# Kernel tuning notes

Hardware: AMD Instinct MI355X
Metric: run time of the kernel (lower is better)

The kernel has to match this reference:

```python
import jax, jax.numpy as jnp
import numpy as np

HEADS = 4
DIM_HEAD = 32
DIM = 128
HIDDEN = HEADS * DIM_HEAD  # 128
LN_EPS = 1e-6


def setup_inputs() -> dict:
    key = jax.random.key(0)
    ks = jax.random.split(key, 4)
    b, X, Y, Z = 4, 32, 32, 32
    x = jax.random.normal(ks[0], (b, X, Y, Z, DIM), dtype=jnp.float32)
    # 1x1x1 convs are pointwise linears: kernel [in, out]
    w_qkv = jax.random.normal(ks[1], (DIM, 3 * HIDDEN), dtype=jnp.float32) * (DIM ** -0.5)
    w_out = jax.random.normal(ks[2], (HIDDEN, DIM), dtype=jnp.float32) * (HIDDEN ** -0.5)
    b_out = jax.random.normal(ks[3], (DIM,), dtype=jnp.float32) * 0.02
    ln_scale = jnp.ones((DIM,), dtype=jnp.float32)
    ln_bias = jnp.zeros((DIM,), dtype=jnp.float32)
    return {"x": x, "w_qkv": w_qkv, "w_out": w_out, "b_out": b_out,
            "ln_scale": ln_scale, "ln_bias": ln_bias}


def reference(x, w_qkv, w_out, b_out, ln_scale, ln_bias):
    b, X, Y, Z, c = x.shape
    n = X * Y * Z
    scale = DIM_HEAD ** (-0.5)

    # 1x1x1 conv (no bias) == pointwise matmul over channels
    qkv = jnp.einsum('bxyzc,cd->bxyzd', x, w_qkv)  # [b,X,Y,Z,3*hidden]
    q, k, v = jnp.split(qkv, 3, axis=-1)

    # rearrange 'b x y z (h c) -> b h c n'
    def to_bhcn(t):
        return t.reshape(b, n, HEADS, DIM_HEAD).transpose(0, 2, 3, 1)

    q, k, v = to_bhcn(q), to_bhcn(k), to_bhcn(v)

    q = jax.nn.softmax(q, axis=-2) * scale   # softmax over feature dim d
    k = jax.nn.softmax(k, axis=-1)           # softmax over token dim n

    context = jnp.einsum('bhdn,bhcn->bhdc', k, v)   # [b,h,d,c] small d=c=32
    out = jnp.einsum('bhde,bhdn->bhen', context, q) # [b,h,e,n]

    # rearrange 'b h c n -> b x y z (h c)' (cubic volume, matching original)
    out = out.transpose(0, 3, 1, 2).reshape(b, X, Y, Z, HIDDEN)

    # final 1x1x1 conv with bias
    out = jnp.einsum('bxyzh,hc->bxyzc', out, w_out) + b_out

    # LayerNorm over last axis (flax default eps=1e-6, with scale+bias)
    mu = jnp.mean(out, axis=-1, keepdims=True)
    var = jnp.mean(jnp.square(out - mu), axis=-1, keepdims=True)
    out = (out - mu) * jax.lax.rsqrt(var + LN_EPS) * ln_scale + ln_bias
    return out
```

## Files before the change

### kernel.cpp

```cpp
#include <hip/hip_runtime.h>
#include <hip/hip_bf16.h>

typedef _Float16 f16;
typedef _Float16 f16x4 __attribute__((ext_vector_type(4)));
typedef _Float16 f16x8 __attribute__((ext_vector_type(8)));
typedef float f32x4 __attribute__((ext_vector_type(4)));

#define MFMA(a, b, c) __builtin_amdgcn_mfma_f32_16x16x32_f16((a), (b), (c), 0, 0, 0)

#define BB 4
#define NPOS 32768
#define HH 4
#define NBLK 1024
#define NBLK3 2048
#define STATB 2304
#define LDP 136

__device__ __forceinline__ f16x8 ldx8(const float* p) {
  float4 a = *(const float4*)p;
  float4 b = *(const float4*)(p + 4);
  return (f16x8){(f16)a.x, (f16)a.y, (f16)a.z, (f16)a.w,
                 (f16)b.x, (f16)b.y, (f16)b.z, (f16)b.w};
}

__global__ __launch_bounds__(256)
void la_k0_prep(const float* __restrict__ wqkv, f16* __restrict__ wkvF,
                f16* __restrict__ wqF) {
  const int g0 = blockIdx.x * 256 + threadIdx.x;
  for (int i = g0; i < 32768; i += 16384) {
    int j = i & 7, l = (i >> 3) & 63, ks = (i >> 9) & 3, nt = (i >> 11) & 3,
        h = i >> 13;
    int n = 16 * nt + (l & 15);
    int c = 32 * ks + 8 * (l >> 4) + j;
    int col = (n < 32) ? (128 + h * 32 + n) : (256 + h * 32 + (n - 32));
    wkvF[i] = (f16)wqkv[c * 384 + col];
  }
  {
    int i = g0;
    int j = i & 7, l = (i >> 3) & 63, ks = (i >> 9) & 3, a = (i >> 11) & 1,
        h = i >> 12;
    int row = l & 15;
    int n = 8 * (row >> 2) + 4 * a + (row & 3);
    int c = 32 * ks + 8 * (l >> 4) + j;
    wqF[i] = (f16)wqkv[c * 384 + h * 32 + n];
  }
}

__global__ __launch_bounds__(256, 4)
void la_k1_stats(const float* __restrict__ x, const f16* __restrict__ wkvF,
                 char* __restrict__ stats) {
  const int blk = blockIdx.x, t = threadIdx.x;
  const int w = t >> 6, l = t & 63, lg = l >> 4, ln = l & 15;

  __shared__ __align__(16) f16 EV[2][64 * LDP];

  const float* xb = x + (size_t)blk * (128 * 128);
  f16x8 xf[2][4];
#pragma unroll
  for (int mi = 0; mi < 2; ++mi)
#pragma unroll
    for (int ks = 0; ks < 4; ++ks)
      xf[mi][ks] = ldx8(xb + (32 * w + 16 * mi + ln) * 128 + 32 * ks + 8 * lg);

  const f32x4 Z4 = {0.f, 0.f, 0.f, 0.f};

  auto logits = [&](int h, f32x4 (&acc)[2][4]) {
#pragma unroll
    for (int mi = 0; mi < 2; ++mi)
#pragma unroll
      for (int nt = 0; nt < 4; ++nt) acc[mi][nt] = Z4;
#pragma unroll
    for (int ks = 0; ks < 4; ++ks) {
#pragma unroll
      for (int nt = 0; nt < 4; ++nt) {
        f16x8 bf = *(const f16x8*)(wkvF + (((h * 4 + nt) * 4 + ks) << 9) + l * 8);
        acc[0][nt] = MFMA(xf[0][ks], bf, acc[0][nt]);
        acc[1][nt] = MFMA(xf[1][ks], bf, acc[1][nt]);
      }
    }
  };

  auto phaseA = [&](int h, f32x4 (&acc)[2][4]) {
    f16* E = (f16*)EV[h & 1];
    float sl[2] = {0.f, 0.f};
#pragma unroll
    for (int nt = 0; nt < 2; ++nt)
#pragma unroll
      for (int mi = 0; mi < 2; ++mi) {
        float e0 = __expf(acc[mi][nt][0]);
        float e1 = __expf(acc[mi][nt][1]);
        float e2 = __expf(acc[mi][nt][2]);
        float e3 = __expf(acc[mi][nt][3]);
        sl[nt] += (e0 + e1) + (e2 + e3);
        *(f16x4*)&E[(16 * nt + ln) * LDP + 32 * w + 16 * mi + 4 * lg] =
            (f16x4){(f16)e0, (f16)e1, (f16)e2, (f16)e3};
        f32x4 vv = acc[mi][nt + 2];
        *(f16x4*)&E[(32 + 16 * nt + ln) * LDP + 32 * w + 16 * mi + 4 * lg] =
            (f16x4){(f16)vv[0], (f16)vv[1], (f16)vv[2], (f16)vv[3]};
      }
#pragma unroll
    for (int nt = 0; nt < 2; ++nt) {
      sl[nt] += __shfl_xor(sl[nt], 16);
      sl[nt] += __shfl_xor(sl[nt], 32);
    }
    f16* sp = (f16*)(stats + (size_t)(blk * HH + h) * STATB + 2048);
    if (lg == 0) {
      sp[ln * 4 + w] = (f16)sl[0];
      sp[(16 + ln) * 4 + w] = (f16)sl[1];
    }
  };

  auto phaseB = [&](int h) {
    __syncthreads();
    const f16* E = (const f16*)EV[h & 1];
    const int tm = w >> 1, tn = w & 1;
    f32x4 tacc = Z4;
#pragma unroll
    for (int ks = 0; ks < 4; ++ks) {
      f16x8 ea = *(const f16x8*)&E[(16 * tm + ln) * LDP + 32 * ks + 8 * lg];
      f16x8 vb = *(const f16x8*)&E[(32 + 16 * tn + ln) * LDP + 32 * ks + 8 * lg];
      tacc = MFMA(ea, vb, tacc);
    }
    f16* tp = (f16*)(stats + (size_t)(blk * HH + h) * STATB);
#pragma unroll
    for (int r = 0; r < 4; ++r)
      tp[(16 * tm + 4 * lg + r) * 32 + 16 * tn + ln] = (f16)tacc[r];
  };

  f32x4 accA[2][4], accB[2][4];
  logits(0, accA);
  phaseA(0, accA); logits(1, accB); phaseB(0);
  phaseA(1, accB); logits(2, accA); phaseB(1);
  phaseA(2, accA); logits(3, accB); phaseB(2);
  phaseA(3, accB); phaseB(3);
}

__global__ __launch_bounds__(256)
void la_k2_combine(const char* __restrict__ stats, f16* __restrict__ ctxN) {
  const int gid = blockIdx.x;
  const int bh = gid >> 5, d = gid & 31;
  const int b = bh >> 2, h = bh & 3;
  const int t = threadIdx.x, w = t >> 6, l = t & 63;
  const int c = t & 31, grp = t >> 5;
  __shared__ float redt[4][32];
  __shared__ float reds[4];

  float sg = 0.f, tc = 0.f;
  for (int i = grp; i < 256; i += 8) {
    const char* ub = stats + (size_t)((b * 256 + i) * HH + h) * STATB;
    tc += (float)((const f16*)ub)[d * 32 + c];
    f16x4 s4 = *(const f16x4*)(ub + 2048 + d * 8);
    sg += ((float)s4[0] + (float)s4[1]) + ((float)s4[2] + (float)s4[3]);
  }
  tc += __shfl_xor(tc, 32);
  sg += __shfl_xor(sg, 32);
  if (l < 32) redt[w][l] = tc;
  if (l == 0) reds[w] = sg;
  __syncthreads();
  if (t < 32) {
    float tt = (redt[0][t] + redt[1][t]) + (redt[2][t] + redt[3][t]);
    float ss = (reds[0] + reds[1]) + (reds[2] + reds[3]);
    ctxN[((size_t)bh * 32 + d) * 32 + t] = (f16)(tt / ss);
  }
}

__global__ __launch_bounds__(256)
void la_k2b_fold(const f16* __restrict__ ctxN, const float* __restrict__ wout,
                 f16* __restrict__ GTF) {
  const int b = blockIdx.x, t = threadIdx.x;
  const int h = t >> 6, l = t & 63, lg = l >> 4, ln = l & 15;
  const f32x4 Z4 = {0.f, 0.f, 0.f, 0.f};

  const f16* cb = ctxN + (size_t)((b * HH + h) * 32) * 32;
  f16x8 bfrag[2];
#pragma unroll
  for (int nt = 0; nt < 2; ++nt)
    bfrag[nt] = *(const f16x8*)(cb + (16 * nt + ln) * 32 + 8 * lg);

  f16* gf = GTF + (size_t)b * 16384;
#pragma unroll
  for (int mt = 0; mt < 8; ++mt) {
    f16x8 af;
#pragma unroll
    for (int j = 0; j < 8; ++j)
      af[j] = (f16)wout[(32 * h + 8 * lg + j) * 128 + 16 * mt + ln];
#pragma unroll
    for (int nt = 0; nt < 2; ++nt) {
      f32x4 acc = MFMA(af, bfrag[nt], Z4);
#pragma unroll
      for (int r = 0; r < 4; ++r) {
        int dsub = 16 * nt + ln;
        gf[((h * 8 + mt) << 9) + (16 * (dsub >> 3) + 4 * lg + r) * 8 + (dsub & 7)] =
            (f16)acc[r];
      }
    }
  }
}

__global__ __launch_bounds__(256, 2)
void la_k3_out(const float* __restrict__ x, const f16* __restrict__ wqF,
               const f16* __restrict__ GTF, const float* __restrict__ bout,
               const float* __restrict__ lns, const float* __restrict__ lnb,
               float* __restrict__ out) {
  const int blk = blockIdx.x, t = threadIdx.x;
  const int w = t >> 6, l = t & 63, lg = l >> 4, ln = l & 15;
  const int b = blk >> 9;
  const int p0 = blk * 64 + 16 * w;

  const float* xb = x + (size_t)p0 * 128;
  f16x8 xf[4];
#pragma unroll
  for (int ks = 0; ks < 4; ++ks)
    xf[ks] = ldx8(xb + ln * 128 + 32 * ks + 8 * lg);

  const f32x4 Z4 = {0.f, 0.f, 0.f, 0.f};
  const f16* gf = GTF + (size_t)b * 16384;

  f16x8 gA[8], gB[8];
#pragma unroll
  for (int nc = 0; nc < 8; ++nc)
    gA[nc] = *(const f16x8*)(gf + ((0 * 8 + nc) << 9) + l * 8);

  f32x4 y[8];
#pragma unroll
  for (int nc = 0; nc < 8; ++nc) y[nc] = Z4;

  auto qlog = [&](int h, f32x4 (&qa)[2]) {
    qa[0] = Z4;
    qa[1] = Z4;
#pragma unroll
    for (int ks = 0; ks < 4; ++ks) {
      f16x8 a0 = *(const f16x8*)(wqF + (((h * 2 + 0) * 4 + ks) << 9) + l * 8);
      f16x8 a1 = *(const f16x8*)(wqF + (((h * 2 + 1) * 4 + ks) << 9) + l * 8);
      qa[0] = MFMA(a0, xf[ks], qa[0]);
      qa[1] = MFMA(a1, xf[ks], qa[1]);
    }
  };

  auto consume = [&](f32x4 (&qa)[2], f16x8& af) {
    float s = 0.f;
#pragma unroll
    for (int mt = 0; mt < 2; ++mt)
#pragma unroll
      for (int r = 0; r < 4; ++r) {
        qa[mt][r] = __expf(qa[mt][r]);
        s += qa[mt][r];
      }
    s += __shfl_xor(s, 16);
    s += __shfl_xor(s, 32);
    const float inv = 0.17677669529663688f / s;
    af = (f16x8){(f16)(qa[0][0] * inv), (f16)(qa[0][1] * inv),
                 (f16)(qa[0][2] * inv), (f16)(qa[0][3] * inv),
                 (f16)(qa[1][0] * inv), (f16)(qa[1][1] * inv),
                 (f16)(qa[1][2] * inv), (f16)(qa[1][3] * inv)};
  };

  auto prefetch = [&](int h, f16x8 (&g)[8]) {
#pragma unroll
    for (int nc = 0; nc < 8; ++nc)
      g[nc] = *(const f16x8*)(gf + (((h * 8 + nc) << 9) + l * 8));
  };

  auto ymfma = [&](f16x8 (&g)[8], f16x8& af) {
#pragma unroll
    for (int nc = 0; nc < 8; ++nc) y[nc] = MFMA(g[nc], af, y[nc]);
  };

  f32x4 qaA[2], qaB[2];
  f16x8 afA, afB;
  qlog(0, qaA); qlog(1, qaB);
  consume(qaA, afA);
  prefetch(1, gB); ymfma(gA, afA); qlog(2, qaA); consume(qaB, afB);
  prefetch(2, gA); ymfma(gB, afB); qlog(3, qaB); consume(qaA, afA);
  prefetch(3, gB); ymfma(gA, afA); consume(qaB, afB);
  ymfma(gB, afB);

#pragma unroll
  for (int nc = 0; nc < 8; ++nc) {
    f32x4 bb = *(const f32x4*)(bout + 16 * nc + 4 * lg);
    y[nc] += bb;
  }

  float s = 0.f;
#pragma unroll
  for (int nc = 0; nc < 8; ++nc)
    s += (y[nc][0] + y[nc][1]) + (y[nc][2] + y[nc][3]);
  s += __shfl_xor(s, 16);
  s += __shfl_xor(s, 32);
  const float mean = s * (1.f / 128.f);
  float v = 0.f;
#pragma unroll
  for (int nc = 0; nc < 8; ++nc)
#pragma unroll
    for (int r = 0; r < 4; ++r) {
      float dv = y[nc][r] - mean;
      v = fmaf(dv, dv, v);
    }
  v += __shfl_xor(v, 16);
  v += __shfl_xor(v, 32);
  const float inv = rsqrtf(v * (1.f / 128.f) + 1e-6f);

  float* op = out + (size_t)(p0 + ln) * 128;
#pragma unroll
  for (int nc = 0; nc < 8; ++nc) {
    f32x4 sv = *(const f32x4*)(lns + 16 * nc + 4 * lg);
    f32x4 b2 = *(const f32x4*)(lnb + 16 * nc + 4 * lg);
    f32x4 o4;
#pragma unroll
    for (int r = 0; r < 4; ++r)
      o4[r] = (y[nc][r] - mean) * inv * sv[r] + b2[r];
    *(f32x4*)(op + 16 * nc + 4 * lg) = o4;
  }
}

extern "C" void kernel_launch(void* const* d_in, const int* in_sizes, int n_in,
                              void* d_out, int out_size, void* d_ws, size_t ws_size,
                              hipStream_t stream) {
  const float* x = (const float*)d_in[0];
  const float* w_qkv = (const float*)d_in[1];
  const float* w_out = (const float*)d_in[2];
  const float* b_out = (const float*)d_in[3];
  const float* ln_s = (const float*)d_in[4];
  const float* ln_b = (const float*)d_in[5];
  float* out = (float*)d_out;

  char* ws = (char*)d_ws;
  char* stats = ws;
  f16* wkvF = (f16*)(ws + 9437184);
  f16* wqF = (f16*)(ws + 9437184 + 65536);
  f16* GTF = (f16*)(ws + 9437184 + 65536 + 32768);
  f16* ctxN = (f16*)(ws + 9437184 + 65536 + 32768 + 131072);

  la_k0_prep<<<dim3(64), 256, 0, stream>>>(w_qkv, wkvF, wqF);
  la_k1_stats<<<dim3(NBLK), 256, 0, stream>>>(x, wkvF, stats);
  la_k2_combine<<<dim3(512), 256, 0, stream>>>(stats, ctxN);
  la_k2b_fold<<<dim3(BB), 256, 0, stream>>>(ctxN, w_out, GTF);
  la_k3_out<<<dim3(NBLK3), 256, 0, stream>>>(x, wqF, GTF, b_out, ln_s, ln_b, out);
}
```

Before: 87.33 us.

## Use single-wave blocks in output kernel and drop double-buffered G prefetch

The output kernel moves from 256-thread blocks, each covering 64 positions across four waves, to 64-thread single-wave blocks of 16 positions each, so the grid grows fourfold. The explicit double-buffered register prefetch of the folded context/out-projection fragments is removed and each fragment is loaded just before its MFMA. This lowers register pressure and should raise occupancy and scheduling flexibility. The cost is less latency hiding within a wave and more per-block launch overhead.

New measurement: 87.43 us. No clear change (+0.1%).

```diff
diff --git a/kernel.cpp b/kernel.cpp
--- a/kernel.cpp
+++ b/kernel.cpp
@@ -12,7 +12,7 @@
 #define NPOS 32768
 #define HH 4
 #define NBLK 1024
-#define NBLK3 2048
+#define NBLK3 8192
 #define STATB 2304
 #define LDP 136
 
@@ -197,15 +197,15 @@
   }
 }
 
-__global__ __launch_bounds__(256, 2)
+__global__ __launch_bounds__(64)
 void la_k3_out(const float* __restrict__ x, const f16* __restrict__ wqF,
                const f16* __restrict__ GTF, const float* __restrict__ bout,
                const float* __restrict__ lns, const float* __restrict__ lnb,
                float* __restrict__ out) {
-  const int blk = blockIdx.x, t = threadIdx.x;
-  const int w = t >> 6, l = t & 63, lg = l >> 4, ln = l & 15;
-  const int b = blk >> 9;
-  const int p0 = blk * 64 + 16 * w;
+  const int blk = blockIdx.x;
+  const int l = threadIdx.x, lg = l >> 4, ln = l & 15;
+  const int b = blk >> 11;
+  const int p0 = blk * 16;
 
   const float* xb = x + (size_t)p0 * 128;
   f16x8 xf[4];
@@ -215,11 +215,6 @@
 
   const f32x4 Z4 = {0.f, 0.f, 0.f, 0.f};
   const f16* gf = GTF + (size_t)b * 16384;
-
-  f16x8 gA[8], gB[8];
-#pragma unroll
-  for (int nc = 0; nc < 8; ++nc)
-    gA[nc] = *(const f16x8*)(gf + ((0 * 8 + nc) << 9) + l * 8);
 
   f32x4 y[8];
 #pragma unroll
@@ -255,25 +250,21 @@
                  (f16)(qa[1][2] * inv), (f16)(qa[1][3] * inv)};
   };
 
-  auto prefetch = [&](int h, f16x8 (&g)[8]) {
-#pragma unroll
-    for (int nc = 0; nc < 8; ++nc)
-      g[nc] = *(const f16x8*)(gf + (((h * 8 + nc) << 9) + l * 8));
-  };
-
-  auto ymfma = [&](f16x8 (&g)[8], f16x8& af) {
-#pragma unroll
-    for (int nc = 0; nc < 8; ++nc) y[nc] = MFMA(g[nc], af, y[nc]);
+  auto ymfma = [&](int h, f16x8& af) {
+#pragma unroll
+    for (int nc = 0; nc < 8; ++nc) {
+      f16x8 gfr = *(const f16x8*)(gf + (((h * 8 + nc) << 9) + l * 8));
+      y[nc] = MFMA(gfr, af, y[nc]);
+    }
   };
 
   f32x4 qaA[2], qaB[2];
   f16x8 afA, afB;
   qlog(0, qaA); qlog(1, qaB);
-  consume(qaA, afA);
-  prefetch(1, gB); ymfma(gA, afA); qlog(2, qaA); consume(qaB, afB);
-  prefetch(2, gA); ymfma(gB, afB); qlog(3, qaB); consume(qaA, afA);
-  prefetch(3, gB); ymfma(gA, afA); consume(qaB, afB);
-  ymfma(gB, afB);
+  consume(qaA, afA); ymfma(0, afA); qlog(2, qaA);
+  consume(qaB, afB); ymfma(1, afB); qlog(3, qaB);
+  consume(qaA, afA); ymfma(2, afA);
+  consume(qaB, afB); ymfma(3, afB);
 
 #pragma unroll
   for (int nc = 0; nc < 8; ++nc) {
@@ -335,5 +326,5 @@
   la_k1_stats<<<dim3(NBLK), 256, 0, stream>>>(x, wkvF, stats);
   la_k2_combine<<<dim3(512), 256, 0, stream>>>(stats, ctxN);
   la_k2b_fold<<<dim3(BB), 256, 0, stream>>>(ctxN, w_out, GTF);
-  la_k3_out<<<dim3(NBLK3), 256, 0, stream>>>(x, wqF, GTF, b_out, ln_s, ln_b, out);
-}
+  la_k3_out<<<dim3(NBLK3), 64, 0, stream>>>(x, wqF, GTF, b_out, ln_s, ln_b, out);
+}
```
